# Performance work log

Measured on AMD Instinct MI355X. Metric: run time of the kernel, lower is better.

The kernel has to match this reference:

```python
import jax, jax.numpy as jnp
import numpy as np

# --- placement constants (mirror init_kwargs) ---
N = 500_000           # total nodes
M = 450_000           # movable nodes (first M)
NBX = 1024
NBY = 1024
XL = 0.0
YL = 0.0
BSX = 1.0
BSY = 1.0
K = 8                 # max bin span per axis for 'large' nodes (node size < 7*bin)


def setup_inputs() -> dict:
    key = jax.random.key(0)
    k1, k2, k3, k4, k5, k6 = jax.random.split(key, 6)
    # node centers strictly inside the die so large-node windows stay in range
    px = jax.random.uniform(k1, (N,), jnp.float32, 4.0, 1020.0)
    py = jax.random.uniform(k2, (N,), jnp.float32, 4.0, 1020.0)
    pos = jnp.concatenate([px, py])                      # [2N]
    potential_field = jax.random.normal(k3, (NBX, NBY), jnp.float32)
    rho_current = jax.random.uniform(k4, (NBX, NBY), jnp.float32, 0.1, 2.0)
    node_size_x = jax.random.uniform(k5, (N,), jnp.float32, 0.2, 6.0)
    node_size_y = jax.random.uniform(k6, (N,), jnp.float32, 0.2, 6.0)
    return {"pos": pos, "potential_field": potential_field,
            "rho_current": rho_current,
            "node_size_x": node_size_x, "node_size_y": node_size_y}


def _velocity_field(pot, hx, hy):
    # v = -grad(phi): 2nd-order central interior, 1st-order one-sided edges
    vx = -jnp.concatenate([(pot[1:2] - pot[0:1]) / hx,
                           (pot[2:] - pot[:-2]) / (2.0 * hx),
                           (pot[-1:] - pot[-2:-1]) / hx], axis=0)
    vy = -jnp.concatenate([(pot[:, 1:2] - pot[:, 0:1]) / hy,
                           (pot[:, 2:] - pot[:, :-2]) / (2.0 * hy),
                           (pot[:, -1:] - pot[:, -2:-1]) / hy], axis=1)
    return vx, vy


def _axis_window(center, size, lo, bs, nb):
    # per-node K-bin window of overlap lengths along one axis
    left = center - 0.5 * size
    right = center + 0.5 * size
    bmin = jnp.clip(jnp.floor((left - lo) / bs).astype(jnp.int32), 0, nb - 1)
    bmax = jnp.clip(jnp.floor((right - lo) / bs).astype(jnp.int32), 0, nb - 1)
    b = bmin[:, None] + jnp.arange(K, dtype=jnp.int32)        # [M,K]
    bin_left = lo + b.astype(jnp.float32) * bs
    ov = jnp.minimum(right[:, None], bin_left + bs) - jnp.maximum(left[:, None], bin_left)
    ov = jnp.where((b <= bmax[:, None]) & (ov > 0.0), ov, 0.0)
    return jnp.clip(b, 0, nb - 1), ov


def _interpolate_flux(pos, flux_x, flux_y, nsx, nsy):
    pos_x = pos[:N]
    pos_y = pos[N:]
    px = pos_x[:M]
    py = pos_y[:M]
    # --- bilinear path (small nodes) ---
    gx = (px - XL) / BSX
    gy = (py - YL) / BSY
    ix = jnp.clip(jnp.floor(gx).astype(jnp.int32), 0, NBX - 1)
    iy = jnp.clip(jnp.floor(gy).astype(jnp.int32), 0, NBY - 1)
    wx = jnp.clip(gx - ix.astype(jnp.float32), 0.0, 1.0)
    wy = jnp.clip(gy - iy.astype(jnp.float32), 0.0, 1.0)
    ix1 = jnp.clip(ix + 1, 0, NBX - 1)
    iy1 = jnp.clip(iy + 1, 0, NBY - 1)

    def bilerp(f):
        return ((1.0 - wx) * (1.0 - wy) * f[ix, iy] + wx * (1.0 - wy) * f[ix1, iy]
                + (1.0 - wx) * wy * f[ix, iy1] + wx * wy * f[ix1, iy1])

    bil_fx = bilerp(flux_x)
    bil_fy = bilerp(flux_y)
    # --- exact area-weighted path (large nodes), vectorized over K x K window ---
    w = nsx[:M]
    h = nsy[:M]
    bx, ox = _axis_window(px, w, XL, BSX, NBX)                # [M,K]
    by, oy = _axis_window(py, h, YL, BSY, NBY)                # [M,K]
    weights = ox[:, :, None] * oy[:, None, :]                 # [M,K,K] overlap areas
    fx_win = flux_x[bx[:, :, None], by[:, None, :]]           # [M,K,K]
    fy_win = flux_y[bx[:, :, None], by[:, None, :]]
    area = w * h
    safe_area = jnp.maximum(area, 1e-30)
    area_fx = jnp.where(area > 0.0, (fx_win * weights).sum((1, 2)) / safe_area, 0.0)
    area_fy = jnp.where(area > 0.0, (fy_win * weights).sum((1, 2)) / safe_area, 0.0)
    large = (w >= BSX) | (h >= BSY)
    gpx = jnp.where(large, area_fx, bil_fx)
    gpy = jnp.where(large, area_fy, bil_fy)
    grad_pos = jnp.zeros_like(pos)
    grad_pos = grad_pos.at[:M].set(gpx)
    grad_pos = grad_pos.at[N:N + M].set(gpy)
    return grad_pos


def reference(pos, potential_field, rho_current, node_size_x, node_size_y):
    vx, vy = _velocity_field(potential_field, BSX, BSY)
    bin_area = BSX * BSY
    energy = 0.5 * (rho_current * bin_area * (vx * vx + vy * vy)).sum().reshape(1)
    grad_pos = _interpolate_flux(pos, vx, vy, node_size_x, node_size_y)
    return energy, grad_pos
```

## Files before the change

### kernel.cpp

```cpp
#include <hip/hip_runtime.h>
#include <hip/hip_fp16.h>

#define NPART 500000
#define MPART 450000
#define NBXC 1024
#define NBYC 1024
#define NBLK_PART 1954
#define NPARTIAL 512

__device__ __forceinline__ int tidx(int x, int y) {
    return ((((x >> 1) * 128 + (y >> 3)) << 4) + ((x & 1) << 3) + (y & 7));
}

__global__ __launch_bounds__(256) void field_kernel(const float* __restrict__ pot,
                                                    const float* __restrict__ rho,
                                                    __half2* __restrict__ v,
                                                    float* __restrict__ partials) {
    const int idx = blockIdx.x * 256 + threadIdx.x;
    const int x  = idx >> 7;
    const int ty = idx & 127;
    const int j0 = ty << 3;

    const int ip = min(x + 1, NBXC - 1);
    const int im = max(x - 1, 0);
    const float sx = (ip - im == 2) ? 0.5f : 1.0f;

    const float4* pc = reinterpret_cast<const float4*>(pot + x  * NBYC + j0);
    const float4* pu = reinterpret_cast<const float4*>(pot + ip * NBYC + j0);
    const float4* pd = reinterpret_cast<const float4*>(pot + im * NBYC + j0);
    const float4* pr = reinterpret_cast<const float4*>(rho + x  * NBYC + j0);
    float c[8], u[8], d[8], r[8];
    *reinterpret_cast<float4*>(c)     = pc[0]; *reinterpret_cast<float4*>(c + 4) = pc[1];
    *reinterpret_cast<float4*>(u)     = pu[0]; *reinterpret_cast<float4*>(u + 4) = pu[1];
    *reinterpret_cast<float4*>(d)     = pd[0]; *reinterpret_cast<float4*>(d + 4) = pd[1];
    *reinterpret_cast<float4*>(r)     = pr[0]; *reinterpret_cast<float4*>(r + 4) = pr[1];
    const float cl = pot[x * NBYC + max(j0 - 1, 0)];
    const float cr = pot[x * NBYC + min(j0 + 8, NBYC - 1)];

    float vx[8], vy[8];
    #pragma unroll
    for (int k = 0; k < 8; ++k) vx[k] = -(u[k] - d[k]) * sx;
    vy[0] = (j0 == 0) ? -(c[1] - c[0]) : -(c[1] - cl) * 0.5f;
    #pragma unroll
    for (int k = 1; k < 7; ++k) vy[k] = -(c[k + 1] - c[k - 1]) * 0.5f;
    vy[7] = (j0 + 7 == NBYC - 1) ? -(c[7] - c[6]) : -(cr - c[6]) * 0.5f;

    float st[8];
    #pragma unroll
    for (int k = 0; k < 8; ++k)
        st[k] = __builtin_bit_cast(float, __floats2half2_rn(vx[k], vy[k]));
    float4* vp = reinterpret_cast<float4*>(v + ((((x >> 1) * 128 + ty) << 4) + ((x & 1) << 3)));
    vp[0] = *reinterpret_cast<float4*>(st);
    vp[1] = *reinterpret_cast<float4*>(st + 4);

    float e = 0.0f;
    #pragma unroll
    for (int k = 0; k < 8; ++k) e += r[k] * (vx[k] * vx[k] + vy[k] * vy[k]);
    #pragma unroll
    for (int off = 32; off > 0; off >>= 1) e += __shfl_down(e, off, 64);
    __shared__ float smem[4];
    const int lane = threadIdx.x & 63;
    const int wid  = threadIdx.x >> 6;
    if (lane == 0) smem[wid] = e;
    __syncthreads();
    if (threadIdx.x == 0) partials[blockIdx.x] = (smem[0] + smem[1]) + (smem[2] + smem[3]);
}

__global__ __launch_bounds__(256) void particle_kernel(const float* __restrict__ pos,
                                                       const float* __restrict__ nsx,
                                                       const float* __restrict__ nsy,
                                                       const __half2* __restrict__ v,
                                                       const float* __restrict__ partials,
                                                       float* __restrict__ out) {
    __shared__ float smem[4];

    if (blockIdx.x == NBLK_PART) {
        const int t = threadIdx.x;
        float e = partials[t] + partials[t + 256];
        #pragma unroll
        for (int off = 32; off > 0; off >>= 1) e += __shfl_down(e, off, 64);
        const int lane = t & 63;
        const int wid  = t >> 6;
        if (lane == 0) smem[wid] = e;
        __syncthreads();
        if (t == 0) out[0] = 0.5f * ((smem[0] + smem[1]) + (smem[2] + smem[3]));
        return;
    }

    const int i = blockIdx.x * 256 + threadIdx.x;
    if (i >= NPART) return;
    if (i >= MPART) {
        out[1 + i]         = 0.0f;
        out[1 + NPART + i] = 0.0f;
        return;
    }

    const float px = pos[i];
    const float py = pos[NPART + i];
    const float w  = nsx[i];
    const float h  = nsy[i];

    float gpx, gpy;
    const bool large = (w >= 1.0f) || (h >= 1.0f);
    if (!large) {
        int ix = min(max((int)floorf(px), 0), NBXC - 1);
        int iy = min(max((int)floorf(py), 0), NBYC - 1);
        const float wx = fminf(fmaxf(px - (float)ix, 0.0f), 1.0f);
        const float wy = fminf(fmaxf(py - (float)iy, 0.0f), 1.0f);
        const int ix1 = min(ix + 1, NBXC - 1);
        const int iy1 = min(iy + 1, NBYC - 1);
        const float2 f00 = __half22float2(v[tidx(ix,  iy )]);
        const float2 f10 = __half22float2(v[tidx(ix1, iy )]);
        const float2 f01 = __half22float2(v[tidx(ix,  iy1)]);
        const float2 f11 = __half22float2(v[tidx(ix1, iy1)]);
        const float w00 = (1.0f - wx) * (1.0f - wy);
        const float w10 = wx * (1.0f - wy);
        const float w01 = (1.0f - wx) * wy;
        const float w11 = wx * wy;
        gpx = w00 * f00.x + w10 * f10.x + w01 * f01.x + w11 * f11.x;
        gpy = w00 * f00.y + w10 * f10.y + w01 * f01.y + w11 * f11.y;
    } else {
        const float lx = px - 0.5f * w, rx = px + 0.5f * w;
        const float ly = py - 0.5f * h, ry = py + 0.5f * h;
        const int bminx = min(max((int)floorf(lx), 0), NBXC - 1);
        const int bmaxx = min(max((int)floorf(rx), 0), NBXC - 1);
        const int bminy = min(max((int)floorf(ly), 0), NBYC - 1);
        const int bmaxy = min(max((int)floorf(ry), 0), NBYC - 1);
        const int by0 = min(bminy & ~7, NBYC - 16);
        const int ty0 = by0 >> 3;
        const int bx0 = bminx & ~1;
        const bool y2 = (bmaxy - by0) >= 8;

        float oy[16];
        #pragma unroll
        for (int k = 0; k < 16; ++k) {
            const int b = by0 + k;
            const float bl = (float)b;
            float ov = fminf(ry, bl + 1.0f) - fmaxf(ly, bl);
            oy[k] = (b <= bmaxy && ov > 0.0f) ? ov : 0.0f;
        }
        float ox[8];
        #pragma unroll
        for (int k = 0; k < 8; ++k) {
            const int b = bx0 + k;
            const float bl = (float)b;
            float ov = fminf(rx, bl + 1.0f) - fmaxf(lx, bl);
            ov = (b <= bmaxx && ov > 0.0f) ? ov : 0.0f;
            ox[k] = ov;
        }

        const float4 z = make_float4(0.0f, 0.0f, 0.0f, 0.0f);
        float afx = 0.0f, afy = 0.0f;
        #pragma unroll
        for (int p = 0; p < 4; ++p) {
            const float ov0 = ox[2 * p], ov1 = ox[2 * p + 1];
            if (ov0 > 0.0f || ov1 > 0.0f) {
                const float4* tp = reinterpret_cast<const float4*>(
                    v + (((((bx0 >> 1) + p) * 128 + ty0) << 4)));
                float4 A0 = tp[0], A1 = tp[1], B0 = tp[2], B1 = tp[3];
                float4 A2 = z, A3 = z, B2 = z, B3 = z;
                if (y2) { A2 = tp[4]; A3 = tp[5]; B2 = tp[6]; B3 = tp[7]; }
                float sxa = 0.0f, sya = 0.0f, sxb = 0.0f, syb = 0.0f;
                const float* a0 = &A0.x; const float* a1 = &A1.x;
                const float* a2 = &A2.x; const float* a3 = &A3.x;
                const float* b0 = &B0.x; const float* b1 = &B1.x;
                const float* b2 = &B2.x; const float* b3 = &B3.x;
                #pragma unroll
                for (int e = 0; e < 4; ++e) {
                    float2 f;
                    f = __half22float2(__builtin_bit_cast(__half2, a0[e]));
                    sxa += f.x * oy[e];      sya += f.y * oy[e];
                    f = __half22float2(__builtin_bit_cast(__half2, a1[e]));
                    sxa += f.x * oy[4 + e];  sya += f.y * oy[4 + e];
                    f = __half22float2(__builtin_bit_cast(__half2, a2[e]));
                    sxa += f.x * oy[8 + e];  sya += f.y * oy[8 + e];
                    f = __half22float2(__builtin_bit_cast(__half2, a3[e]));
                    sxa += f.x * oy[12 + e]; sya += f.y * oy[12 + e];
                    f = __half22float2(__builtin_bit_cast(__half2, b0[e]));
                    sxb += f.x * oy[e];      syb += f.y * oy[e];
                    f = __half22float2(__builtin_bit_cast(__half2, b1[e]));
                    sxb += f.x * oy[4 + e];  syb += f.y * oy[4 + e];
                    f = __half22float2(__builtin_bit_cast(__half2, b2[e]));
                    sxb += f.x * oy[8 + e];  syb += f.y * oy[8 + e];
                    f = __half22float2(__builtin_bit_cast(__half2, b3[e]));
                    sxb += f.x * oy[12 + e]; syb += f.y * oy[12 + e];
                }
                afx += sxa * ov0 + sxb * ov1;
                afy += sya * ov0 + syb * ov1;
            }
        }
        const float inv = 1.0f / fmaxf(w * h, 1e-30f);
        gpx = afx * inv;
        gpy = afy * inv;
    }
    out[1 + i]         = gpx;
    out[1 + NPART + i] = gpy;
}

extern "C" void kernel_launch(void* const* d_in, const int* in_sizes, int n_in,
                              void* d_out, int out_size, void* d_ws, size_t ws_size,
                              hipStream_t stream) {
    const float* pos = (const float*)d_in[0];
    const float* pot = (const float*)d_in[1];
    const float* rho = (const float*)d_in[2];
    const float* nsx = (const float*)d_in[3];
    const float* nsy = (const float*)d_in[4];
    float* out = (float*)d_out;

    __half2* v      = (__half2*)d_ws;
    float* partials = (float*)((char*)d_ws + (size_t)NBXC * NBYC * sizeof(__half2));

    field_kernel<<<NPARTIAL, 256, 0, stream>>>(pot, rho, v, partials);
    particle_kernel<<<NBLK_PART + 1, 256, 0, stream>>>(pos, nsx, nsy, v, partials, out);
}
```

Baseline: 30.01 us.

## Split velocity tiles into planar fp16 x/y and use fdot2 for window sums

Changes the tiled velocity buffer from interleaved half2 (vx,vy) pairs to separate fp16 planes of vx and vy inside each 2x8 tile. Adjacent y-bins then pack into half2 words, so the large-node overlap sum can use packed fp16 dot-product instructions (v_dot2) against fp16 y-overlap weights instead of unpacking to fp32 and doing scalar FMAs. The aim is fewer ALU instructions in the large-node path. The trade-offs are that y-overlap weights are rounded to fp16, which lowers accuracy, and the bilinear path now needs two scalar half loads per corner instead of one half2 load.

```diff
diff --git a/kernel.cpp b/kernel.cpp
--- a/kernel.cpp
+++ b/kernel.cpp
@@ -5,16 +5,16 @@
 #define MPART 450000
 #define NBXC 1024
 #define NBYC 1024
+#define NPARTIAL 512
 #define NBLK_PART 1954
-#define NPARTIAL 512
-
-__device__ __forceinline__ int tidx(int x, int y) {
-    return ((((x >> 1) * 128 + (y >> 3)) << 4) + ((x & 1) << 3) + (y & 7));
-}
+
+typedef float  fvec4 __attribute__((ext_vector_type(4)));
+typedef _Float16 h2  __attribute__((ext_vector_type(2)));
+
 
 __global__ __launch_bounds__(256) void field_kernel(const float* __restrict__ pot,
                                                     const float* __restrict__ rho,
-                                                    __half2* __restrict__ v,
+                                                    __half* __restrict__ v,
                                                     float* __restrict__ partials) {
     const int idx = blockIdx.x * 256 + threadIdx.x;
     const int x  = idx >> 7;
@@ -25,15 +25,15 @@
     const int im = max(x - 1, 0);
     const float sx = (ip - im == 2) ? 0.5f : 1.0f;
 
-    const float4* pc = reinterpret_cast<const float4*>(pot + x  * NBYC + j0);
-    const float4* pu = reinterpret_cast<const float4*>(pot + ip * NBYC + j0);
-    const float4* pd = reinterpret_cast<const float4*>(pot + im * NBYC + j0);
-    const float4* pr = reinterpret_cast<const float4*>(rho + x  * NBYC + j0);
+    const fvec4* pc = reinterpret_cast<const fvec4*>(pot + x  * NBYC + j0);
+    const fvec4* pu = reinterpret_cast<const fvec4*>(pot + ip * NBYC + j0);
+    const fvec4* pd = reinterpret_cast<const fvec4*>(pot + im * NBYC + j0);
+    const fvec4* pr = reinterpret_cast<const fvec4*>(rho + x  * NBYC + j0);
     float c[8], u[8], d[8], r[8];
-    *reinterpret_cast<float4*>(c)     = pc[0]; *reinterpret_cast<float4*>(c + 4) = pc[1];
-    *reinterpret_cast<float4*>(u)     = pu[0]; *reinterpret_cast<float4*>(u + 4) = pu[1];
-    *reinterpret_cast<float4*>(d)     = pd[0]; *reinterpret_cast<float4*>(d + 4) = pd[1];
-    *reinterpret_cast<float4*>(r)     = pr[0]; *reinterpret_cast<float4*>(r + 4) = pr[1];
+    *reinterpret_cast<fvec4*>(c)     = pc[0]; *reinterpret_cast<fvec4*>(c + 4) = pc[1];
+    *reinterpret_cast<fvec4*>(u)     = pu[0]; *reinterpret_cast<fvec4*>(u + 4) = pu[1];
+    *reinterpret_cast<fvec4*>(d)     = pd[0]; *reinterpret_cast<fvec4*>(d + 4) = pd[1];
+    *reinterpret_cast<fvec4*>(r)     = pr[0]; *reinterpret_cast<fvec4*>(r + 4) = pr[1];
     const float cl = pot[x * NBYC + max(j0 - 1, 0)];
     const float cr = pot[x * NBYC + min(j0 + 8, NBYC - 1)];
 
@@ -45,13 +45,15 @@
     for (int k = 1; k < 7; ++k) vy[k] = -(c[k + 1] - c[k - 1]) * 0.5f;
     vy[7] = (j0 + 7 == NBYC - 1) ? -(c[7] - c[6]) : -(cr - c[6]) * 0.5f;
 
-    float st[8];
-    #pragma unroll
-    for (int k = 0; k < 8; ++k)
-        st[k] = __builtin_bit_cast(float, __floats2half2_rn(vx[k], vy[k]));
-    float4* vp = reinterpret_cast<float4*>(v + ((((x >> 1) * 128 + ty) << 4) + ((x & 1) << 3)));
-    vp[0] = *reinterpret_cast<float4*>(st);
-    vp[1] = *reinterpret_cast<float4*>(st + 4);
+    float stx[4], sty[4];
+    #pragma unroll
+    for (int k = 0; k < 4; ++k) {
+        stx[k] = __builtin_bit_cast(float, __floats2half2_rn(vx[2 * k], vx[2 * k + 1]));
+        sty[k] = __builtin_bit_cast(float, __floats2half2_rn(vy[2 * k], vy[2 * k + 1]));
+    }
+    __half* tp = v + ((((x >> 1) * 128 + ty) << 5) + ((x & 1) << 3));
+    *reinterpret_cast<fvec4*>(tp)      = *reinterpret_cast<fvec4*>(stx);
+    *reinterpret_cast<fvec4*>(tp + 16) = *reinterpret_cast<fvec4*>(sty);
 
     float e = 0.0f;
     #pragma unroll
@@ -66,10 +68,15 @@
     if (threadIdx.x == 0) partials[blockIdx.x] = (smem[0] + smem[1]) + (smem[2] + smem[3]);
 }
 
+__device__ __forceinline__ float2 vload(const __half* __restrict__ v, int x, int y) {
+    const __half* t = v + ((((x >> 1) * 128 + (y >> 3)) << 5) + ((x & 1) << 3) + (y & 7));
+    return make_float2(__half2float(t[0]), __half2float(t[16]));
+}
+
 __global__ __launch_bounds__(256) void particle_kernel(const float* __restrict__ pos,
                                                        const float* __restrict__ nsx,
                                                        const float* __restrict__ nsy,
-                                                       const __half2* __restrict__ v,
+                                                       const __half* __restrict__ v,
                                                        const float* __restrict__ partials,
                                                        float* __restrict__ out) {
     __shared__ float smem[4];
@@ -109,10 +116,10 @@
         const float wy = fminf(fmaxf(py - (float)iy, 0.0f), 1.0f);
         const int ix1 = min(ix + 1, NBXC - 1);
         const int iy1 = min(iy + 1, NBYC - 1);
-        const float2 f00 = __half22float2(v[tidx(ix,  iy )]);
-        const float2 f10 = __half22float2(v[tidx(ix1, iy )]);
-        const float2 f01 = __half22float2(v[tidx(ix,  iy1)]);
-        const float2 f11 = __half22float2(v[tidx(ix1, iy1)]);
+        const float2 f00 = vload(v, ix,  iy );
+        const float2 f10 = vload(v, ix1, iy );
+        const float2 f01 = vload(v, ix,  iy1);
+        const float2 f11 = vload(v, ix1, iy1);
         const float w00 = (1.0f - wx) * (1.0f - wy);
         const float w10 = wx * (1.0f - wy);
         const float w01 = (1.0f - wx) * wy;
@@ -131,13 +138,15 @@
         const int bx0 = bminx & ~1;
         const bool y2 = (bmaxy - by0) >= 8;
 
-        float oy[16];
-        #pragma unroll
-        for (int k = 0; k < 16; ++k) {
-            const int b = by0 + k;
-            const float bl = (float)b;
-            float ov = fminf(ry, bl + 1.0f) - fmaxf(ly, bl);
-            oy[k] = (b <= bmaxy && ov > 0.0f) ? ov : 0.0f;
+        h2 hoy[8];
+        #pragma unroll
+        for (int k = 0; k < 8; ++k) {
+            const int b0 = by0 + 2 * k, b1 = b0 + 1;
+            float o0 = fminf(ry, (float)b0 + 1.0f) - fmaxf(ly, (float)b0);
+            float o1 = fminf(ry, (float)b1 + 1.0f) - fmaxf(ly, (float)b1);
+            o0 = (b0 <= bmaxy && o0 > 0.0f) ? o0 : 0.0f;
+            o1 = (b1 <= bmaxy && o1 > 0.0f) ? o1 : 0.0f;
+            hoy[k] = h2{(_Float16)o0, (_Float16)o1};
         }
         float ox[8];
         #pragma unroll
@@ -145,45 +154,32 @@
             const int b = bx0 + k;
             const float bl = (float)b;
             float ov = fminf(rx, bl + 1.0f) - fmaxf(lx, bl);
-            ov = (b <= bmaxx && ov > 0.0f) ? ov : 0.0f;
-            ox[k] = ov;
+            ox[k] = (b <= bmaxx && ov > 0.0f) ? ov : 0.0f;
         }
 
-        const float4 z = make_float4(0.0f, 0.0f, 0.0f, 0.0f);
+        const fvec4 z = {0.0f, 0.0f, 0.0f, 0.0f};
         float afx = 0.0f, afy = 0.0f;
         #pragma unroll
         for (int p = 0; p < 4; ++p) {
             const float ov0 = ox[2 * p], ov1 = ox[2 * p + 1];
             if (ov0 > 0.0f || ov1 > 0.0f) {
-                const float4* tp = reinterpret_cast<const float4*>(
-                    v + (((((bx0 >> 1) + p) * 128 + ty0) << 4)));
-                float4 A0 = tp[0], A1 = tp[1], B0 = tp[2], B1 = tp[3];
-                float4 A2 = z, A3 = z, B2 = z, B3 = z;
-                if (y2) { A2 = tp[4]; A3 = tp[5]; B2 = tp[6]; B3 = tp[7]; }
-                float sxa = 0.0f, sya = 0.0f, sxb = 0.0f, syb = 0.0f;
-                const float* a0 = &A0.x; const float* a1 = &A1.x;
-                const float* a2 = &A2.x; const float* a3 = &A3.x;
-                const float* b0 = &B0.x; const float* b1 = &B1.x;
-                const float* b2 = &B2.x; const float* b3 = &B3.x;
+                const fvec4* tp = reinterpret_cast<const fvec4*>(
+                    v + (((((bx0 >> 1) + p) * 128 + ty0) << 5)));
+                fvec4 XA0 = tp[0], XB0 = tp[1], YA0 = tp[2], YB0 = tp[3];
+                fvec4 XA1 = z, XB1 = z, YA1 = z, YB1 = z;
+                if (y2) { XA1 = tp[4]; XB1 = tp[5]; YA1 = tp[6]; YB1 = tp[7]; }
+
+                float sxa = 0.0f, sxb = 0.0f, sya = 0.0f, syb = 0.0f;
                 #pragma unroll
                 for (int e = 0; e < 4; ++e) {
-                    float2 f;
-                    f = __half22float2(__builtin_bit_cast(__half2, a0[e]));
-                    sxa += f.x * oy[e];      sya += f.y * oy[e];
-                    f = __half22float2(__builtin_bit_cast(__half2, a1[e]));
-                    sxa += f.x * oy[4 + e];  sya += f.y * oy[4 + e];
-                    f = __half22float2(__builtin_bit_cast(__half2, a2[e]));
-                    sxa += f.x * oy[8 + e];  sya += f.y * oy[8 + e];
-                    f = __half22float2(__builtin_bit_cast(__half2, a3[e]));
-                    sxa += f.x * oy[12 + e]; sya += f.y * oy[12 + e];
-                    f = __half22float2(__builtin_bit_cast(__half2, b0[e]));
-                    sxb += f.x * oy[e];      syb += f.y * oy[e];
-                    f = __half22float2(__builtin_bit_cast(__half2, b1[e]));
-                    sxb += f.x * oy[4 + e];  syb += f.y * oy[4 + e];
-                    f = __half22float2(__builtin_bit_cast(__half2, b2[e]));
-                    sxb += f.x * oy[8 + e];  syb += f.y * oy[8 + e];
-                    f = __half22float2(__builtin_bit_cast(__half2, b3[e]));
-                    sxb += f.x * oy[12 + e]; syb += f.y * oy[12 + e];
+                    sxa = __builtin_amdgcn_fdot2(__builtin_bit_cast(h2, XA0[e]), hoy[e],     sxa, false);
+                    sxb = __builtin_amdgcn_fdot2(__builtin_bit_cast(h2, XB0[e]), hoy[e],     sxb, false);
+                    sya = __builtin_amdgcn_fdot2(__builtin_bit_cast(h2, YA0[e]), hoy[e],     sya, false);
+                    syb = __builtin_amdgcn_fdot2(__builtin_bit_cast(h2, YB0[e]), hoy[e],     syb, false);
+                    sxa = __builtin_amdgcn_fdot2(__builtin_bit_cast(h2, XA1[e]), hoy[4 + e], sxa, false);
+                    sxb = __builtin_amdgcn_fdot2(__builtin_bit_cast(h2, XB1[e]), hoy[4 + e], sxb, false);
+                    sya = __builtin_amdgcn_fdot2(__builtin_bit_cast(h2, YA1[e]), hoy[4 + e], sya, false);
+                    syb = __builtin_amdgcn_fdot2(__builtin_bit_cast(h2, YB1[e]), hoy[4 + e], syb, false);
                 }
                 afx += sxa * ov0 + sxb * ov1;
                 afy += sya * ov0 + syb * ov1;
@@ -207,8 +203,8 @@
     const float* nsy = (const float*)d_in[4];
     float* out = (float*)d_out;
 
-    __half2* v      = (__half2*)d_ws;
-    float* partials = (float*)((char*)d_ws + (size_t)NBXC * NBYC * sizeof(__half2));
+    __half* v       = (__half*)d_ws;
+    float* partials = (float*)((char*)d_ws + (size_t)2 * NBXC * NBYC * sizeof(__half));
 
     field_kernel<<<NPARTIAL, 256, 0, stream>>>(pot, rho, v, partials);
     particle_kernel<<<NBLK_PART + 1, 256, 0, stream>>>(pos, nsx, nsy, v, partials, out);
```

New measurement: 29.93 us. About the same (-0.3%).
